# Kernel tuning notes

Measured on AMD Instinct MI355X. Metric: run time of the kernel, lower is better.

The kernel has to match this reference:

```python
import jax, jax.numpy as jnp
import numpy as np

B, T, H = 2, 2048, 1024
EXPAND, N = 2, 16
DIN = H * EXPAND  # 2048
EPS = 1e-6


def rmsnorm(x, w):
    var = jnp.mean(x * x, axis=-1, keepdims=True)
    return x * jax.lax.rsqrt(var + EPS) * w


def setup_inputs() -> dict:
    key = jax.random.key(0)
    ks = jax.random.split(key, 9)
    s_h = 1.0 / np.sqrt(H)
    s_d = 1.0 / np.sqrt(DIN)
    return {
        "x": jax.random.normal(ks[0], (B, T, H), jnp.float32),
        "norm_w": jnp.ones((H,), jnp.float32),
        "in_proj_w": jax.random.normal(ks[1], (H, 2 * DIN), jnp.float32) * s_h,
        "A_proj_w": jax.random.normal(ks[2], (DIN, DIN), jnp.float32) * s_d,
        "A_proj_b": jax.random.normal(ks[3], (DIN,), jnp.float32) * 0.02,
        "A_base": jnp.log(jnp.arange(1, N + 1, dtype=jnp.float32)),
        "B_proj_w": jax.random.normal(ks[4], (DIN, N), jnp.float32) * s_d,
        "C_proj_w": jax.random.normal(ks[5], (DIN, N), jnp.float32) * s_d,
        "D": jnp.ones((DIN,), jnp.float32),
        "out_proj_w": jax.random.normal(ks[6], (DIN, H), jnp.float32) * s_d,
    }


def liquid_scan(x_in, a_mod, a_base, B_in, C_in):
    # x_in, a_mod: [B,T,DIN]; B_in, C_in: [B,T,N]; a_base: [N]
    def step(h, inp):
        a_t, b_t, c_t, x_t = inp  # [B,DIN], [B,N], [B,N], [B,DIN]
        # h: [B, DIN, N]
        h = (a_t[:, :, None] * a_base) * h + b_t[:, None, :] * x_t[:, :, None]
        y_t = jnp.einsum('bdn,bn->bd', h, c_t)
        return h, y_t

    h0 = jnp.zeros((x_in.shape[0], DIN, N), x_in.dtype)
    xs = (jnp.swapaxes(a_mod, 0, 1), jnp.swapaxes(B_in, 0, 1),
          jnp.swapaxes(C_in, 0, 1), jnp.swapaxes(x_in, 0, 1))
    _, ys = jax.lax.scan(step, h0, xs)  # ys: [T,B,DIN]
    return jnp.swapaxes(ys, 0, 1)


def reference(x, norm_w, in_proj_w, A_proj_w, A_proj_b, A_base, B_proj_w, C_proj_w, D, out_proj_w):
    residual = x
    xn = rmsnorm(x, norm_w)
    xz = xn @ in_proj_w                      # [B,T,2*DIN]
    x_in, z = jnp.split(xz, 2, axis=-1)
    x_in = jax.nn.silu(x_in)
    a_mod = jax.nn.sigmoid(x_in @ A_proj_w + A_proj_b)  # [B,T,DIN]
    a_base = jax.nn.sigmoid(A_base)                      # [N]
    B_in = x_in @ B_proj_w                               # [B,T,N]
    C_in = x_in @ C_proj_w                               # [B,T,N]
    y = liquid_scan(x_in, a_mod, a_base, B_in, C_in)     # [B,T,DIN]
    y = (y + D * x_in) * jax.nn.silu(z)
    return residual + y @ out_proj_w
```

## Files before the change

kernel.cpp:

```cpp
#include <hip/hip_runtime.h>
#include <hip/hip_fp16.h>
#include <cstdint>

#define B_    2
#define T_    2048
#define H_    1024
#define DIN_  2048
#define NS_   16
#define M_    (B_*T_)
#define NCHUNK 64
#define LCHUNK 32

using bf16x8 = __attribute__((ext_vector_type(8))) short;
using f32x4  = __attribute__((ext_vector_type(4))) float;

__device__ __forceinline__ unsigned short f2bf(float f) {
    union { float f; uint32_t u; } x; x.f = f;
    uint32_t u = x.u;
    uint32_t r = (u + 0x7fffu + ((u >> 16) & 1u)) >> 16;
    return (unsigned short)r;
}
__device__ __forceinline__ float bf2f(unsigned short h) {
    union { uint32_t u; float f; } x; x.u = ((uint32_t)h) << 16;
    return x.f;
}
__device__ __forceinline__ float sigm(float v) { return 1.0f / (1.0f + expf(-v)); }
__device__ __forceinline__ float silu(float v) { return v / (1.0f + expf(-v)); }

__device__ __forceinline__ void gload_lds16(const void* g, void* l) {
    __builtin_amdgcn_global_load_lds(
        (__attribute__((address_space(1))) void*)(void*)g,
        (__attribute__((address_space(3))) void*)l, 16, 0, 0);
}

__global__ __launch_bounds__(256)
void prep_all(const float* __restrict__ in_proj, const float* __restrict__ A_proj,
              const float* __restrict__ out_proj,
              const float* __restrict__ x, const float* __restrict__ norm_w,
              unsigned short* __restrict__ inT, unsigned short* __restrict__ W2,
              unsigned short* __restrict__ outT, unsigned short* __restrict__ xnh) {
    int bid = blockIdx.x;
    int tid = threadIdx.x;
    __shared__ float tile[32][33];
    __shared__ float red[4];
    if (bid >= 10240) {
        int row = bid - 10240;
        const float4* xr = (const float4*)(x + (size_t)row * H_);
        float4 v = xr[tid];
        float ss = v.x * v.x + v.y * v.y + v.z * v.z + v.w * v.w;
#pragma unroll
        for (int o = 32; o > 0; o >>= 1) ss += __shfl_down(ss, o, 64);
        int lane = tid & 63, wv = tid >> 6;
        if (lane == 0) red[wv] = ss;
        __syncthreads();
        float tot = red[0] + red[1] + red[2] + red[3];
        float rstd = rsqrtf(tot / (float)H_ + 1e-6f);
        const float4* wr = (const float4*)norm_w;
        float4 w4 = wr[tid];
        size_t o = (size_t)row * H_ + tid * 4;
        *(ushort4*)&xnh[o] = make_ushort4(f2bf(v.x * rstd * w4.x), f2bf(v.y * rstd * w4.y),
                                          f2bf(v.z * rstd * w4.z), f2bf(v.w * rstd * w4.w));
        return;
    }
    const float* src; unsigned short* dst; int K, N, l;
    if (bid < 4096)      { src = in_proj;  dst = inT;  K = 1024; N = 4096; l = bid; }
    else if (bid < 8192) { src = A_proj;   dst = W2;   K = 2048; N = 2048; l = bid - 4096; }
    else                 { src = out_proj; dst = outT; K = 2048; N = 1024; l = bid - 8192; }
    int ntiles = N >> 5;
    int n0 = (l % ntiles) * 32, k0 = (l / ntiles) * 32;
    int tx = tid & 31, ty = tid >> 5;
#pragma unroll
    for (int i = 0; i < 32; i += 8)
        tile[ty + i][tx] = src[(size_t)(k0 + ty + i) * N + (n0 + tx)];
    __syncthreads();
    int sx = (tid & 15) * 2;
    int sy = tid >> 4;
#pragma unroll
    for (int i = 0; i < 32; i += 16) {
        int n = sy + i;
        float v0 = tile[sx][n], v1 = tile[sx + 1][n];
        size_t o = (size_t)(n0 + n) * K + (k0 + sx);
        *(ushort2*)&dst[o] = make_ushort2(f2bf(v0), f2bf(v1));
    }
}

template <int EPI, int BM, int BN>
__global__ __launch_bounds__(512, (BM == 128) ? 4 : 2)
void gemm8p(const unsigned short* __restrict__ Aa, const unsigned short* __restrict__ Bw,
            int K,
            float* __restrict__ out0,
            unsigned short* __restrict__ oh, unsigned short* __restrict__ oz,
            const float* __restrict__ aux, __half* __restrict__ oha) {
    constexpr int AU   = (BM / 16) * 2;
    constexpr int BU   = (BN / 16) * 2;
    constexpr int BUFU = AU + BU;
    constexpr int MF   = BM / 2 / 16;
    constexpr int NF   = BN / 4 / 16;
    constexpr int PH   = (NF == 4) ? 2 : 1;
    constexpr int NP   = NF / PH;
    constexpr int SPWK = BUFU / 8;
    constexpr int SPG  = SPWK / 2;
    constexpr int SPP  = SPG / PH;
    __shared__ unsigned short sm[2 * BUFU * 512];
    const int tid  = threadIdx.x;
    const int lane = tid & 63;
    const int wid  = tid >> 6;
    const int wm   = wid >> 2;
    const int wn   = wid & 3;

    const int gx   = gridDim.x;
    const int nwg  = gx * gridDim.y;
    const int orig = blockIdx.y * gx + blockIdx.x;
    const int qq   = nwg >> 3;
    const int lid  = (orig & 7) * qq + (orig >> 3);
    const int bm   = (lid / gx) * BM;
    const int bn   = (lid % gx) * BN;

    const int srow  = lane >> 2;
    const int sgran = (lane & 3) ^ ((lane >> 3) & 3);
    const unsigned short* gpp[SPWK];
    int lofs_[SPWK];
#pragma unroll
    for (int g = 0; g < 2; ++g)
#pragma unroll
        for (int i = 0; i < SPG; ++i) {
            int cn = wid * SPG + i;
            const unsigned short* src;
            int u;
            if (cn < AU / 2) { u = cn * 2 + g;             src = Aa + (size_t)(bm + cn * 16 + srow) * K; }
            else { int bc = cn - AU / 2; u = AU + bc * 2 + g; src = Bw + (size_t)(bn + bc * 16 + srow) * K; }
            gpp[g * SPG + i]   = src + g * 32 + sgran * 8;
            lofs_[g * SPG + i] = u * 512;
        }

    const int nt = K >> 6;
#pragma unroll
    for (int j = 0; j < SPWK; ++j) gload_lds16(gpp[j], &sm[lofs_[j]]);

    const int fro = (lane & 15) * 32 + (((lane >> 4) ^ ((lane >> 1) & 3)) * 8);

    f32x4 acc[MF][NF] = {};
    for (int kt = 0; kt < nt; ++kt) {
        const unsigned short* sb = &sm[(kt & 1) * (BUFU * 512)];
        unsigned short*       db = &sm[((kt + 1) & 1) * (BUFU * 512)];
        const bool pf = (kt + 1 < nt);
        bf16x8 af[MF];
#pragma unroll
        for (int ks = 0; ks < 2; ++ks) {
            if (ks == 1 && kt == nt - 1) {
                asm volatile("s_waitcnt vmcnt(0)" ::: "memory");
            } else {
                if constexpr (SPG == 4)      asm volatile("s_waitcnt vmcnt(4)" ::: "memory");
                else if constexpr (SPG == 3) asm volatile("s_waitcnt vmcnt(3)" ::: "memory");
                else                         asm volatile("s_waitcnt vmcnt(2)" ::: "memory");
            }
            __builtin_amdgcn_s_barrier();
            __builtin_amdgcn_sched_barrier(0);
#pragma unroll
            for (int ph = 0; ph < PH; ++ph) {
                if (ph) {
                    __builtin_amdgcn_s_barrier();
                    __builtin_amdgcn_sched_barrier(0);
                }
                if (ph == 0) {
#pragma unroll
                    for (int mf = 0; mf < MF; ++mf)
                        af[mf] = *(const bf16x8*)&sb[((wm * MF + mf) * 2 + ks) * 512 + fro];
                }
                bf16x8 bf8[NP];
#pragma unroll
                for (int j = 0; j < NP; ++j) {
                    int nfg = ph * NP + j;
                    bf8[j] = *(const bf16x8*)&sb[(AU + (wn * NF + nfg) * 2 + ks) * 512 + fro];
                }
                if (pf) {
#pragma unroll
                    for (int j = 0; j < SPP; ++j) {
                        int s = (ks * PH + ph) * SPP + j;
                        gload_lds16(gpp[s] + (size_t)(kt + 1) * 64, db + lofs_[s]);
                    }
                }
                __builtin_amdgcn_s_setprio(1);
#pragma unroll
                for (int mf = 0; mf < MF; ++mf)
#pragma unroll
                    for (int j = 0; j < NP; ++j)
                        acc[mf][ph * NP + j] = __builtin_amdgcn_mfma_f32_16x16x32_bf16(
                            af[mf], bf8[j], acc[mf][ph * NP + j], 0, 0, 0);
                __builtin_amdgcn_s_setprio(0);
            }
        }
    }

#pragma unroll
    for (int mf = 0; mf < MF; ++mf)
#pragma unroll
        for (int nf = 0; nf < NF; ++nf) {
            int col  = bn + (wn * NF + nf) * 16 + (lane & 15);
            int row0 = bm + (wm * MF + mf) * 16 + ((lane >> 4) << 2);
#pragma unroll
            for (int r = 0; r < 4; ++r) {
                int row = row0 + r;
                float v = acc[mf][nf][r];
                if (EPI == 0) {
                    float s = silu(v);
                    if (col < DIN_) oh[(size_t)row * DIN_ + col] = f2bf(s);
                    else            oz[(size_t)row * DIN_ + (col - DIN_)] = f2bf(s);
                } else if (EPI == 1) {
                    oha[(size_t)row * DIN_ + col] = __float2half(sigm(v + aux[col]));
                } else {
                    out0[(size_t)row * H_ + col] = v + aux[(size_t)row * H_ + col];
                }
            }
        }
}

#define KT_ 512
__global__ __launch_bounds__(256)
void bc_proj(const unsigned short* __restrict__ xh,
             const float* __restrict__ Bw, const float* __restrict__ Cw,
             float* __restrict__ Bout, float* __restrict__ Cout) {
    __shared__ float wB[KT_][17];
    __shared__ float wC[KT_][17];
    const int m0  = blockIdx.x * 16;
    const int tid = threadIdx.x;
    const int r   = tid >> 4;
    const int j   = tid & 15;
    float ab[16], ac[16];
#pragma unroll
    for (int i = 0; i < 16; ++i) { ab[i] = 0.f; ac[i] = 0.f; }

    for (int kt = 0; kt < DIN_; kt += KT_) {
        if (kt) __syncthreads();
        const float4* bs = (const float4*)(Bw + (size_t)kt * 16);
        const float4* cs = (const float4*)(Cw + (size_t)kt * 16);
#pragma unroll
        for (int i = 0; i < 8; ++i) {
            int idx = i * 256 + tid;
            int kk = idx >> 2, c4 = (idx & 3) * 4;
            float4 vb = bs[idx], vc = cs[idx];
            wB[kk][c4 + 0] = vb.x; wB[kk][c4 + 1] = vb.y; wB[kk][c4 + 2] = vb.z; wB[kk][c4 + 3] = vb.w;
            wC[kk][c4 + 0] = vc.x; wC[kk][c4 + 1] = vc.y; wC[kk][c4 + 2] = vc.z; wC[kk][c4 + 3] = vc.w;
        }
        __syncthreads();
        const unsigned short* xr = xh + (size_t)(m0 + r) * DIN_ + kt;
#pragma unroll 4
        for (int kk = 0; kk < 32; ++kk) {
            int kl = kk * 16 + j;
            float x = bf2f(xr[kl]);
#pragma unroll
            for (int c = 0; c < 16; ++c) {
                ab[c] = fmaf(x, wB[kl][c], ab[c]);
                ac[c] = fmaf(x, wC[kl][c], ac[c]);
            }
        }
    }
#pragma unroll
    for (int i = 0; i < 16; ++i) {
#pragma unroll
        for (int m = 8; m > 0; m >>= 1) {
            ab[i] += __shfl_xor(ab[i], m, 64);
            ac[i] += __shfl_xor(ac[i], m, 64);
        }
    }
    if (j == 0) {
#pragma unroll
        for (int i = 0; i < 16; ++i) {
            Bout[(size_t)(m0 + r) * 16 + i] = ab[i];
            Cout[(size_t)(m0 + r) * 16 + i] = ac[i];
        }
    }
}

__global__ __launch_bounds__(256)
void scan_phase1(const __half* __restrict__ amod, const unsigned short* __restrict__ xh,
                 const float* __restrict__ Bin, const float* __restrict__ Abase,
                 float* __restrict__ P, float* __restrict__ S) {
    int d = blockIdx.x * 256 + threadIdx.x;
    int c = blockIdx.y;
    int b = blockIdx.z;
    float ab[16];
#pragma unroll
    for (int n = 0; n < 16; ++n) ab[n] = sigm(Abase[n]);
    float p[16], s[16];
#pragma unroll
    for (int n = 0; n < 16; ++n) { p[n] = 1.0f; s[n] = 0.0f; }
    int t0 = c * LCHUNK;
    for (int tt = 0; tt < LCHUNK; ++tt) {
        size_t mrow = (size_t)(b * T_ + t0 + tt);
        float a = __half2float(amod[mrow * DIN_ + d]);
        float x = bf2f(xh[mrow * DIN_ + d]);
        const float4* bt4 = (const float4*)(Bin + mrow * 16);
        float4 q0 = bt4[0], q1 = bt4[1], q2 = bt4[2], q3 = bt4[3];
        float bt[16];
        bt[0]=q0.x; bt[1]=q0.y; bt[2]=q0.z; bt[3]=q0.w;
        bt[4]=q1.x; bt[5]=q1.y; bt[6]=q1.z; bt[7]=q1.w;
        bt[8]=q2.x; bt[9]=q2.y; bt[10]=q2.z; bt[11]=q2.w;
        bt[12]=q3.x; bt[13]=q3.y; bt[14]=q3.z; bt[15]=q3.w;
#pragma unroll
        for (int n = 0; n < 16; ++n) {
            float dk = a * ab[n];
            p[n] *= dk;
            s[n] = fmaf(dk, s[n], bt[n] * x);
        }
    }
    size_t base = ((size_t)(b * NCHUNK + c) << 15) + (size_t)d * 16;
    float4* P4 = (float4*)(P + base);
    float4* S4 = (float4*)(S + base);
#pragma unroll
    for (int j = 0; j < 4; ++j) {
        P4[j] = make_float4(p[4*j], p[4*j+1], p[4*j+2], p[4*j+3]);
        S4[j] = make_float4(s[4*j], s[4*j+1], s[4*j+2], s[4*j+3]);
    }
}

__global__ __launch_bounds__(256)
void scan_phase2(const float* __restrict__ P, const float* __restrict__ S,
                 float* __restrict__ H0) {
    int idx = blockIdx.x * 256 + threadIdx.x;
    int b = idx >> 15;
    int dn = idx & 32767;
    float g = 0.f;
    for (int c = 0; c < NCHUNK; ++c) {
        size_t base = ((size_t)(b * NCHUNK + c) << 15) + dn;
        H0[base] = g;
        g = fmaf(P[base], g, S[base]);
    }
}

__global__ __launch_bounds__(256)
void scan_phase3(const __half* __restrict__ amod, const unsigned short* __restrict__ xh,
                 const float* __restrict__ Bin, const float* __restrict__ Cin,
                 const float* __restrict__ Abase, const float* __restrict__ H0,
                 const float* __restrict__ Dp, const unsigned short* __restrict__ szh,
                 unsigned short* __restrict__ yh) {
    int d = blockIdx.x * 256 + threadIdx.x;
    int c = blockIdx.y;
    int b = blockIdx.z;
    float ab[16];
#pragma unroll
    for (int n = 0; n < 16; ++n) ab[n] = sigm(Abase[n]);
    float h[16];
    size_t hbase = ((size_t)(b * NCHUNK + c) << 15) + (size_t)d * 16;
    const float4* H4 = (const float4*)(H0 + hbase);
#pragma unroll
    for (int j = 0; j < 4; ++j) {
        float4 t4 = H4[j];
        h[j*4] = t4.x; h[j*4+1] = t4.y; h[j*4+2] = t4.z; h[j*4+3] = t4.w;
    }
    float Dd = Dp[d];
    int t0 = c * LCHUNK;
    for (int tt = 0; tt < LCHUNK; ++tt) {
        size_t mrow = (size_t)(b * T_ + t0 + tt);
        float a = __half2float(amod[mrow * DIN_ + d]);
        float x = bf2f(xh[mrow * DIN_ + d]);
        const float4* bt4 = (const float4*)(Bin + mrow * 16);
        const float4* ct4 = (const float4*)(Cin + mrow * 16);
        float4 q0 = bt4[0], q1 = bt4[1], q2 = bt4[2], q3 = bt4[3];
        float4 r0 = ct4[0], r1 = ct4[1], r2 = ct4[2], r3 = ct4[3];
        float bt[16], ct[16];
        bt[0]=q0.x; bt[1]=q0.y; bt[2]=q0.z; bt[3]=q0.w;
        bt[4]=q1.x; bt[5]=q1.y; bt[6]=q1.z; bt[7]=q1.w;
        bt[8]=q2.x; bt[9]=q2.y; bt[10]=q2.z; bt[11]=q2.w;
        bt[12]=q3.x; bt[13]=q3.y; bt[14]=q3.z; bt[15]=q3.w;
        ct[0]=r0.x; ct[1]=r0.y; ct[2]=r0.z; ct[3]=r0.w;
        ct[4]=r1.x; ct[5]=r1.y; ct[6]=r1.z; ct[7]=r1.w;
        ct[8]=r2.x; ct[9]=r2.y; ct[10]=r2.z; ct[11]=r2.w;
        ct[12]=r3.x; ct[13]=r3.y; ct[14]=r3.z; ct[15]=r3.w;
        float y = 0.f;
#pragma unroll
        for (int n = 0; n < 16; ++n) {
            float dk = a * ab[n];
            h[n] = fmaf(dk, h[n], bt[n] * x);
            y = fmaf(h[n], ct[n], y);
        }
        float val = (y + Dd * x) * bf2f(szh[mrow * DIN_ + d]);
        yh[mrow * DIN_ + d] = f2bf(val);
    }
}

extern "C" void kernel_launch(void* const* d_in, const int* in_sizes, int n_in,
                              void* d_out, int out_size, void* d_ws, size_t ws_size,
                              hipStream_t stream) {
    const float* x          = (const float*)d_in[0];
    const float* norm_w     = (const float*)d_in[1];
    const float* in_proj_w  = (const float*)d_in[2];
    const float* A_proj_w   = (const float*)d_in[3];
    const float* A_proj_b   = (const float*)d_in[4];
    const float* A_base     = (const float*)d_in[5];
    const float* B_proj_w   = (const float*)d_in[6];
    const float* C_proj_w   = (const float*)d_in[7];
    const float* Dp         = (const float*)d_in[8];
    const float* out_proj_w = (const float*)d_in[9];
    float* out = (float*)d_out;

    char* ws = (char*)d_ws;
    size_t off = 0;
    auto alloc = [&](size_t bytes) -> char* {
        char* p = ws + off;
        off += (bytes + 255) & ~(size_t)255;
        return p;
    };
    unsigned short* inT  = (unsigned short*)alloc((size_t)4096 * 1024 * 2);
    unsigned short* W2   = (unsigned short*)alloc((size_t)2048 * 2048 * 2);
    unsigned short* outT = (unsigned short*)alloc((size_t)1024 * 2048 * 2);
    unsigned short* xnh  = (unsigned short*)alloc((size_t)M_ * H_ * 2);
    unsigned short* xinh = (unsigned short*)alloc((size_t)M_ * DIN_ * 2);
    unsigned short* szh  = (unsigned short*)alloc((size_t)M_ * DIN_ * 2);
    __half* amod  = (__half*)alloc((size_t)M_ * DIN_ * 2);
    float* Bin    = (float*)alloc((size_t)M_ * 16 * 4);
    float* Cin    = (float*)alloc((size_t)M_ * 16 * 4);
    float* Pw     = (float*)alloc((size_t)B_ * NCHUNK * DIN_ * NS_ * 4);
    float* Sw     = (float*)alloc((size_t)B_ * NCHUNK * DIN_ * NS_ * 4);
    float* H0w    = (float*)alloc((size_t)B_ * NCHUNK * DIN_ * NS_ * 4);
    unsigned short* yh = (unsigned short*)alloc((size_t)M_ * DIN_ * 2);
    (void)ws_size;

    prep_all<<<14336, 256, 0, stream>>>(in_proj_w, A_proj_w, out_proj_w, x, norm_w,
                                        inT, W2, outT, xnh);

    gemm8p<0, 256, 256><<<dim3(4096 / 256, M_ / 256), 512, 0, stream>>>(
        xnh, inT, 1024, nullptr, xinh, szh, nullptr, nullptr);

    gemm8p<1, 128, 128><<<dim3(2048 / 128, M_ / 128), 512, 0, stream>>>(
        xinh, W2, 2048, nullptr, nullptr, nullptr, A_proj_b, amod);

    bc_proj<<<M_ / 16, 256, 0, stream>>>(xinh, B_proj_w, C_proj_w, Bin, Cin);

    scan_phase1<<<dim3(DIN_ / 256, NCHUNK, B_), 256, 0, stream>>>(amod, xinh, Bin, A_base, Pw, Sw);
    scan_phase2<<<(B_ * DIN_ * NS_) / 256, 256, 0, stream>>>(Pw, Sw, H0w);
    scan_phase3<<<dim3(DIN_ / 256, NCHUNK, B_), 256, 0, stream>>>(
        amod, xinh, Bin, Cin, A_base, H0w, Dp, szh, yh);

    gemm8p<2, 128, 128><<<dim3(1024 / 128, M_ / 128), 512, 0, stream>>>(
        yh, outT, 2048, out, nullptr, nullptr, x, nullptr);
}
```

Before: 233.4 us.

## Fuse A-projection GEMM and B/C projection into one heterogeneous kernel launch

Replaces the separate A_proj GEMM launch and the bc_proj launch with one kernel, g2_bc. Blocks 0-255 run a dedicated 256x128-tile bf16 MFMA GEMM with a swizzled block mapping and a sigmoid epilogue. Blocks 256-383 compute the B/C projections with a smaller K tile. This removes one launch and lets the small projection work run concurrently with the big GEMM. The cost is less flexible occupancy, a larger GEMM tile (fewer blocks), and the projection blocks competing for CU slots.

Result: slower. 240.7 us (+3.1%).

```diff
diff --git a/kernel.cpp b/kernel.cpp
--- a/kernel.cpp
+++ b/kernel.cpp
@@ -90,7 +90,7 @@
             int K,
             float* __restrict__ out0,
             unsigned short* __restrict__ oh, unsigned short* __restrict__ oz,
-            const float* __restrict__ aux, __half* __restrict__ oha) {
+            const float* __restrict__ aux) {
     constexpr int AU   = (BM / 16) * 2;
     constexpr int BU   = (BN / 16) * 2;
     constexpr int BUFU = AU + BU;
@@ -206,8 +206,6 @@
                     float s = silu(v);
                     if (col < DIN_) oh[(size_t)row * DIN_ + col] = f2bf(s);
                     else            oz[(size_t)row * DIN_ + (col - DIN_)] = f2bf(s);
-                } else if (EPI == 1) {
-                    oha[(size_t)row * DIN_ + col] = __float2half(sigm(v + aux[col]));
                 } else {
                     out0[(size_t)row * H_ + col] = v + aux[(size_t)row * H_ + col];
                 }
@@ -215,61 +213,152 @@
         }
 }
 
-#define KT_ 512
-__global__ __launch_bounds__(256)
-void bc_proj(const unsigned short* __restrict__ xh,
-             const float* __restrict__ Bw, const float* __restrict__ Cw,
-             float* __restrict__ Bout, float* __restrict__ Cout) {
-    __shared__ float wB[KT_][17];
-    __shared__ float wC[KT_][17];
-    const int m0  = blockIdx.x * 16;
+__global__ __launch_bounds__(512, 2)
+void g2_bc(const unsigned short* __restrict__ Aa, const unsigned short* __restrict__ Bw,
+           const float* __restrict__ aux, __half* __restrict__ oha,
+           const float* __restrict__ Bpw, const float* __restrict__ Cpw,
+           float* __restrict__ Bout, float* __restrict__ Cout) {
+    constexpr int K    = 2048;
+    constexpr int AU   = 32, BU = 16, BUFU = 48;
+    constexpr int MF   = 8, NF = 2;
+    constexpr int SPWK = 6, SPG = 3;
+    __shared__ __align__(16) char pool[2 * BUFU * 512 * 2];
+    const int bid = blockIdx.x;
     const int tid = threadIdx.x;
-    const int r   = tid >> 4;
-    const int j   = tid & 15;
-    float ab[16], ac[16];
-#pragma unroll
-    for (int i = 0; i < 16; ++i) { ab[i] = 0.f; ac[i] = 0.f; }
-
-    for (int kt = 0; kt < DIN_; kt += KT_) {
-        if (kt) __syncthreads();
-        const float4* bs = (const float4*)(Bw + (size_t)kt * 16);
-        const float4* cs = (const float4*)(Cw + (size_t)kt * 16);
-#pragma unroll
-        for (int i = 0; i < 8; ++i) {
-            int idx = i * 256 + tid;
-            int kk = idx >> 2, c4 = (idx & 3) * 4;
-            float4 vb = bs[idx], vc = cs[idx];
-            wB[kk][c4 + 0] = vb.x; wB[kk][c4 + 1] = vb.y; wB[kk][c4 + 2] = vb.z; wB[kk][c4 + 3] = vb.w;
-            wC[kk][c4 + 0] = vc.x; wC[kk][c4 + 1] = vc.y; wC[kk][c4 + 2] = vc.z; wC[kk][c4 + 3] = vc.w;
-        }
-        __syncthreads();
-        const unsigned short* xr = xh + (size_t)(m0 + r) * DIN_ + kt;
+
+    if (bid >= 256) {
+        float (*wB)[17] = (float(*)[17])pool;
+        float (*wC)[17] = (float(*)[17])(pool + 256 * 17 * 4);
+        const int m0 = (bid - 256) * 32;
+        const int r  = tid >> 4;
+        const int j  = tid & 15;
+        float ab[16], ac[16];
+#pragma unroll
+        for (int i = 0; i < 16; ++i) { ab[i] = 0.f; ac[i] = 0.f; }
+        for (int kt = 0; kt < DIN_; kt += 256) {
+            if (kt) __syncthreads();
+            const float4* bs = (const float4*)(Bpw + (size_t)kt * 16);
+            const float4* cs = (const float4*)(Cpw + (size_t)kt * 16);
+#pragma unroll
+            for (int i = 0; i < 2; ++i) {
+                int idx = i * 512 + tid;
+                int kk = idx >> 2, c4 = (idx & 3) * 4;
+                float4 vb = bs[idx], vc = cs[idx];
+                wB[kk][c4 + 0] = vb.x; wB[kk][c4 + 1] = vb.y; wB[kk][c4 + 2] = vb.z; wB[kk][c4 + 3] = vb.w;
+                wC[kk][c4 + 0] = vc.x; wC[kk][c4 + 1] = vc.y; wC[kk][c4 + 2] = vc.z; wC[kk][c4 + 3] = vc.w;
+            }
+            __syncthreads();
+            const unsigned short* xr = Aa + (size_t)(m0 + r) * DIN_ + kt;
 #pragma unroll 4
-        for (int kk = 0; kk < 32; ++kk) {
-            int kl = kk * 16 + j;
-            float x = bf2f(xr[kl]);
-#pragma unroll
-            for (int c = 0; c < 16; ++c) {
-                ab[c] = fmaf(x, wB[kl][c], ab[c]);
-                ac[c] = fmaf(x, wC[kl][c], ac[c]);
-            }
-        }
-    }
-#pragma unroll
-    for (int i = 0; i < 16; ++i) {
-#pragma unroll
-        for (int m = 8; m > 0; m >>= 1) {
-            ab[i] += __shfl_xor(ab[i], m, 64);
-            ac[i] += __shfl_xor(ac[i], m, 64);
-        }
-    }
-    if (j == 0) {
+            for (int kk = 0; kk < 16; ++kk) {
+                int kl = kk * 16 + j;
+                float x = bf2f(xr[kl]);
+#pragma unroll
+                for (int c = 0; c < 16; ++c) {
+                    ab[c] = fmaf(x, wB[kl][c], ab[c]);
+                    ac[c] = fmaf(x, wC[kl][c], ac[c]);
+                }
+            }
+        }
 #pragma unroll
         for (int i = 0; i < 16; ++i) {
-            Bout[(size_t)(m0 + r) * 16 + i] = ab[i];
-            Cout[(size_t)(m0 + r) * 16 + i] = ac[i];
-        }
-    }
+#pragma unroll
+            for (int m = 8; m > 0; m >>= 1) {
+                ab[i] += __shfl_xor(ab[i], m, 64);
+                ac[i] += __shfl_xor(ac[i], m, 64);
+            }
+        }
+        if (j == 0) {
+#pragma unroll
+            for (int i = 0; i < 16; ++i) {
+                Bout[(size_t)(m0 + r) * 16 + i] = ab[i];
+                Cout[(size_t)(m0 + r) * 16 + i] = ac[i];
+            }
+        }
+        return;
+    }
+
+    unsigned short* sm = (unsigned short*)pool;
+    const int lane = tid & 63;
+    const int wid  = tid >> 6;
+    const int wm   = wid >> 2;
+    const int wn   = wid & 3;
+    const int orig = bid;
+    const int lid  = (orig & 7) * 32 + (orig >> 3);
+    const int bm   = (lid / 16) * 256;
+    const int bn   = (lid % 16) * 128;
+
+    const int srow  = lane >> 2;
+    const int sgran = (lane & 3) ^ ((lane >> 3) & 3);
+    const unsigned short* gpp[SPWK];
+    int lofs_[SPWK];
+#pragma unroll
+    for (int g = 0; g < 2; ++g)
+#pragma unroll
+        for (int i = 0; i < SPG; ++i) {
+            int cn = wid * SPG + i;
+            const unsigned short* src;
+            int u;
+            if (cn < AU / 2) { u = cn * 2 + g;             src = Aa + (size_t)(bm + cn * 16 + srow) * K; }
+            else { int bc2 = cn - AU / 2; u = AU + bc2 * 2 + g; src = Bw + (size_t)(bn + bc2 * 16 + srow) * K; }
+            gpp[g * SPG + i]   = src + g * 32 + sgran * 8;
+            lofs_[g * SPG + i] = u * 512;
+        }
+
+    const int nt = K >> 6;
+#pragma unroll
+    for (int j = 0; j < SPWK; ++j) gload_lds16(gpp[j], &sm[lofs_[j]]);
+
+    const int fro = (lane & 15) * 32 + (((lane >> 4) ^ ((lane >> 1) & 3)) * 8);
+
+    f32x4 acc[MF][NF] = {};
+    for (int kt = 0; kt < nt; ++kt) {
+        const unsigned short* sb = &sm[(kt & 1) * (BUFU * 512)];
+        unsigned short*       db = &sm[((kt + 1) & 1) * (BUFU * 512)];
+        const bool pf = (kt + 1 < nt);
+        bf16x8 af[MF];
+#pragma unroll
+        for (int ks = 0; ks < 2; ++ks) {
+            if (ks == 1 && kt == nt - 1) asm volatile("s_waitcnt vmcnt(0)" ::: "memory");
+            else                         asm volatile("s_waitcnt vmcnt(3)" ::: "memory");
+            __builtin_amdgcn_s_barrier();
+            __builtin_amdgcn_sched_barrier(0);
+#pragma unroll
+            for (int mf = 0; mf < MF; ++mf)
+                af[mf] = *(const bf16x8*)&sb[((wm * MF + mf) * 2 + ks) * 512 + fro];
+            bf16x8 bf8[NF];
+#pragma unroll
+            for (int j = 0; j < NF; ++j)
+                bf8[j] = *(const bf16x8*)&sb[(AU + (wn * NF + j) * 2 + ks) * 512 + fro];
+            if (pf) {
+#pragma unroll
+                for (int j = 0; j < SPG; ++j) {
+                    int s = ks * SPG + j;
+                    gload_lds16(gpp[s] + (size_t)(kt + 1) * 64, db + lofs_[s]);
+                }
+            }
+            __builtin_amdgcn_s_setprio(1);
+#pragma unroll
+            for (int mf = 0; mf < MF; ++mf)
+#pragma unroll
+                for (int j = 0; j < NF; ++j)
+                    acc[mf][j] = __builtin_amdgcn_mfma_f32_16x16x32_bf16(af[mf], bf8[j], acc[mf][j], 0, 0, 0);
+            __builtin_amdgcn_s_setprio(0);
+        }
+    }
+
+#pragma unroll
+    for (int mf = 0; mf < MF; ++mf)
+#pragma unroll
+        for (int nf = 0; nf < NF; ++nf) {
+            int col  = bn + (wn * NF + nf) * 16 + (lane & 15);
+            int row0 = bm + (wm * MF + mf) * 16 + ((lane >> 4) << 2);
+#pragma unroll
+            for (int r = 0; r < 4; ++r) {
+                int row = row0 + r;
+                oha[(size_t)row * DIN_ + col] = __float2half(sigm(acc[mf][nf][r] + aux[col]));
+            }
+        }
 }
 
 __global__ __launch_bounds__(256)
@@ -420,12 +509,10 @@
                                         inT, W2, outT, xnh);
 
     gemm8p<0, 256, 256><<<dim3(4096 / 256, M_ / 256), 512, 0, stream>>>(
-        xnh, inT, 1024, nullptr, xinh, szh, nullptr, nullptr);
-
-    gemm8p<1, 128, 128><<<dim3(2048 / 128, M_ / 128), 512, 0, stream>>>(
-        xinh, W2, 2048, nullptr, nullptr, nullptr, A_proj_b, amod);
-
-    bc_proj<<<M_ / 16, 256, 0, stream>>>(xinh, B_proj_w, C_proj_w, Bin, Cin);
+        xnh, inT, 1024, nullptr, xinh, szh, nullptr);
+
+    g2_bc<<<384, 512, 0, stream>>>(xinh, W2, A_proj_b, amod,
+                                   B_proj_w, C_proj_w, Bin, Cin);
 
     scan_phase1<<<dim3(DIN_ / 256, NCHUNK, B_), 256, 0, stream>>>(amod, xinh, Bin, A_base, Pw, Sw);
     scan_phase2<<<(B_ * DIN_ * NS_) / 256, 256, 0, stream>>>(Pw, Sw, H0w);
@@ -433,5 +520,5 @@
         amod, xinh, Bin, Cin, A_base, H0w, Dp, szh, yh);
 
     gemm8p<2, 128, 128><<<dim3(1024 / 128, M_ / 128), 512, 0, stream>>>(
-        yh, outT, 2048, out, nullptr, nullptr, x, nullptr);
-}
+        yh, outT, 2048, out, nullptr, nullptr, x);
+}
```
